# Performance work log

Hardware: AMD Instinct MI355X
Metric: run time of the kernel (lower is better)

## Reference

```python
import jax, jax.numpy as jnp
import numpy as np

B, S, H = 16, 4096, 512

def setup_inputs() -> dict:
    key = jax.random.key(0)
    k1, k2, k3, k4, k5 = jax.random.split(key, 5)
    hidden = jax.random.normal(k1, (B, H), dtype=jnp.float32)
    encoder_outputs = jax.random.normal(k2, (B, S, 2 * H), dtype=jnp.float32)
    # nn.Linear(3H, H): weight [H, 3H], bias [H]
    W_attn = jax.random.normal(k3, (H, 3 * H), dtype=jnp.float32) * (1.0 / np.sqrt(3 * H))
    b_attn = jax.random.normal(k4, (H,), dtype=jnp.float32) * 0.01
    v = jax.random.normal(k5, (H,), dtype=jnp.float32)
    return {"hidden": hidden, "encoder_outputs": encoder_outputs,
            "W_attn": W_attn, "b_attn": b_attn, "v": v}

def reference(hidden, encoder_outputs, W_attn, b_attn, v):
    src_len = encoder_outputs.shape[1]
    # [B, S, H] broadcast of decoder hidden, concat with encoder outputs -> [B, S, 3H]
    h_rep = jnp.broadcast_to(hidden[:, None, :], (hidden.shape[0], src_len, hidden.shape[1]))
    combined = jnp.concatenate([h_rep, encoder_outputs], axis=2)
    energy = jnp.tanh(jnp.einsum('bsf,hf->bsh', combined, W_attn) + b_attn)
    attention = jnp.einsum('bsh,h->bs', energy, v)  # bmm(v, energy.T) squeezed
    return jax.nn.softmax(attention, axis=1)
```

## Files before the change

### kernel.cpp

```cpp
#include <hip/hip_runtime.h>

typedef __attribute__((ext_vector_type(4))) float f32x4;
typedef __attribute__((ext_vector_type(8))) short bf16x8;
typedef __attribute__((ext_vector_type(4))) short bf16x4;

#define MEMBAR() asm volatile("" ::: "memory")

__device__ __forceinline__ unsigned short f2bf(float f) {
  unsigned int u = __builtin_bit_cast(unsigned int, f);
  u += 0x7FFFu + ((u >> 16) & 1u);
  return (unsigned short)(u >> 16);
}

__global__ __launch_bounds__(256) void k_prep(
    const float* __restrict__ W, const float* __restrict__ hidden,
    const float* __restrict__ bias, unsigned short* __restrict__ W2t,
    float* __restrict__ P) {
  __shared__ float hsh[512];
  const int bid = blockIdx.x;
  const int tid = threadIdx.x;
  if (bid < 256) {
    const int id = bid * 256 + tid;
    const int kk8 = (id & 3) * 8;
    const int h = (id >> 2) & 511;
    const int kb = id >> 11;
    const float* src = W + (long)h * 1536 + 512 + kb * 32 + kk8;
    float4 a = *reinterpret_cast<const float4*>(src);
    float4 c = *reinterpret_cast<const float4*>(src + 4);
    union { unsigned short u[8]; bf16x8 v; } o;
    o.u[0] = f2bf(a.x); o.u[1] = f2bf(a.y); o.u[2] = f2bf(a.z); o.u[3] = f2bf(a.w);
    o.u[4] = f2bf(c.x); o.u[5] = f2bf(c.y); o.u[6] = f2bf(c.z); o.u[7] = f2bf(c.w);
    *reinterpret_cast<bf16x8*>(W2t + (long)kb * 16384 + h * 32 + kk8) = o.v;
  } else {
    const int bid2 = bid - 256;
    const int b = bid2 >> 1;
    const int h = (bid2 & 1) * 256 + tid;
    for (int i = tid; i < 512; i += 256) hsh[i] = hidden[b * 512 + i];
    __syncthreads();
    const float* wr = W + (long)h * 1536;
    float s = 0.f;
#pragma unroll 4
    for (int f = 0; f < 512; f += 4) {
      float4 wv = *reinterpret_cast<const float4*>(wr + f);
      s += wv.x * hsh[f] + wv.y * hsh[f + 1] + wv.z * hsh[f + 2] + wv.w * hsh[f + 3];
    }
    P[b * 512 + h] = bias[h] + s;
  }
}

__global__ __launch_bounds__(512, 2) void k_main(
    const float* __restrict__ enc, const short* __restrict__ W2t,
    const float* __restrict__ P, const float* __restrict__ v,
    float* __restrict__ logits) {
  __shared__ short As[4][2048];
  __shared__ float attred[64][8];

  const int tid = threadIdx.x;
  const int lane = tid & 63;
  const int w = tid >> 6;
  const int hl = lane & 15, kg = lane >> 4;
  const long rowbase = (long)blockIdx.x * 64;
  const int b = (int)(rowbase >> 12);

  const int r = tid >> 3, c = tid & 7;
  const f32x4* gp = reinterpret_cast<const f32x4*>(enc + (rowbase + r) * 1024) + c;
  const int wr_off = r * 32 + ((((c >> 1) ^ ((r >> 1) & 3)) << 3)) + ((c & 1) << 2);
  const int base_f = hl * 32 + ((kg ^ ((hl >> 1) & 3)) << 3);
  const short* bp = W2t + (w * 64 + hl) * 32 + kg * 8;

  f32x4 acc[4][4];
#pragma unroll
  for (int mi = 0; mi < 4; ++mi)
#pragma unroll
    for (int ni = 0; ni < 4; ++ni) acc[mi][ni] = (f32x4){0.f, 0.f, 0.f, 0.f};

  bf16x8 Ba[4], Bb[4];
  f32x4 rawE, rawO;

#define CVT4W(BUF, RAW) {                                             \
    union { __bf16 h[4]; bf16x4 s; } _u;                              \
    _u.h[0] = (__bf16)(RAW)[0]; _u.h[1] = (__bf16)(RAW)[1];           \
    _u.h[2] = (__bf16)(RAW)[2]; _u.h[3] = (__bf16)(RAW)[3];           \
    *reinterpret_cast<bf16x4*>(&As[(BUF)][wr_off]) = _u.s;            \
  }
#define LOADB(DST, KB) {                                              \
    const short* _k = bp + (KB) * 16384;                              \
    DST[0] = *reinterpret_cast<const bf16x8*>(_k);                    \
    DST[1] = *reinterpret_cast<const bf16x8*>(_k + 512);              \
    DST[2] = *reinterpret_cast<const bf16x8*>(_k + 1024);             \
    DST[3] = *reinterpret_cast<const bf16x8*>(_k + 1536);             \
  }
#define K_ITER(J, RAWIN, RAWOUT, BIN, BOUT, DO_G, DO_B, DO_CVT) {     \
    MEMBAR();                                                         \
    __builtin_amdgcn_s_barrier();                                     \
    MEMBAR();                                                         \
    if (DO_G) RAWOUT = gp[((J) + 2) * 8];                             \
    if (DO_B) LOADB(BOUT, (J) + 1);                                   \
    MEMBAR();                                                         \
    const short* _ab = &As[(J) & 3][0];                               \
    bf16x8 _f0 = *reinterpret_cast<const bf16x8*>(_ab + base_f);      \
    bf16x8 _f1 = *reinterpret_cast<const bf16x8*>(_ab + base_f + 512);\
    bf16x8 _f2 = *reinterpret_cast<const bf16x8*>(_ab + base_f + 1024);\
    bf16x8 _f3 = *reinterpret_cast<const bf16x8*>(_ab + base_f + 1536);\
    acc[0][0] = __builtin_amdgcn_mfma_f32_16x16x32_bf16(_f0, BIN[0], acc[0][0], 0, 0, 0); \
    acc[0][1] = __builtin_amdgcn_mfma_f32_16x16x32_bf16(_f0, BIN[1], acc[0][1], 0, 0, 0); \
    acc[0][2] = __builtin_amdgcn_mfma_f32_16x16x32_bf16(_f0, BIN[2], acc[0][2], 0, 0, 0); \
    acc[0][3] = __builtin_amdgcn_mfma_f32_16x16x32_bf16(_f0, BIN[3], acc[0][3], 0, 0, 0); \
    acc[1][0] = __builtin_amdgcn_mfma_f32_16x16x32_bf16(_f1, BIN[0], acc[1][0], 0, 0, 0); \
    acc[1][1] = __builtin_amdgcn_mfma_f32_16x16x32_bf16(_f1, BIN[1], acc[1][1], 0, 0, 0); \
    acc[1][2] = __builtin_amdgcn_mfma_f32_16x16x32_bf16(_f1, BIN[2], acc[1][2], 0, 0, 0); \
    acc[1][3] = __builtin_amdgcn_mfma_f32_16x16x32_bf16(_f1, BIN[3], acc[1][3], 0, 0, 0); \
    acc[2][0] = __builtin_amdgcn_mfma_f32_16x16x32_bf16(_f2, BIN[0], acc[2][0], 0, 0, 0); \
    acc[2][1] = __builtin_amdgcn_mfma_f32_16x16x32_bf16(_f2, BIN[1], acc[2][1], 0, 0, 0); \
    acc[2][2] = __builtin_amdgcn_mfma_f32_16x16x32_bf16(_f2, BIN[2], acc[2][2], 0, 0, 0); \
    acc[2][3] = __builtin_amdgcn_mfma_f32_16x16x32_bf16(_f2, BIN[3], acc[2][3], 0, 0, 0); \
    acc[3][0] = __builtin_amdgcn_mfma_f32_16x16x32_bf16(_f3, BIN[0], acc[3][0], 0, 0, 0); \
    acc[3][1] = __builtin_amdgcn_mfma_f32_16x16x32_bf16(_f3, BIN[1], acc[3][1], 0, 0, 0); \
    acc[3][2] = __builtin_amdgcn_mfma_f32_16x16x32_bf16(_f3, BIN[2], acc[3][2], 0, 0, 0); \
    acc[3][3] = __builtin_amdgcn_mfma_f32_16x16x32_bf16(_f3, BIN[3], acc[3][3], 0, 0, 0); \
    if (DO_CVT) CVT4W(((J) + 1) & 3, RAWIN);                          \
    asm volatile("s_waitcnt lgkmcnt(0)" ::: "memory");                \
  }

  {
    f32x4 raw0 = gp[0];
    CVT4W(0, raw0);
  }
  rawO = gp[8];
  LOADB(Ba, 0);
  __syncthreads();

#pragma unroll 1
  for (int p = 0; p < 15; ++p) {
    const int j = p * 2;
    K_ITER(j,     rawO, rawE, Ba, Bb, 1, 1, 1);
    K_ITER(j + 1, rawE, rawO, Bb, Ba, 1, 1, 1);
  }
  K_ITER(30, rawO, rawE, Ba, Bb, 0, 1, 1);
  K_ITER(31, rawE, rawO, Bb, Ba, 0, 0, 0);

#undef K_ITER
#undef LOADB
#undef CVT4W

  float part[4][4];
#pragma unroll
  for (int mi = 0; mi < 4; ++mi)
#pragma unroll
    for (int rr = 0; rr < 4; ++rr) part[mi][rr] = 0.f;

#pragma unroll
  for (int ni = 0; ni < 4; ++ni) {
    const int h = w * 64 + ni * 16 + hl;
    const float ph = P[b * 512 + h];
    const float vh = v[h];
#pragma unroll
    for (int mi = 0; mi < 4; ++mi)
#pragma unroll
      for (int rr = 0; rr < 4; ++rr) {
        float x = acc[mi][ni][rr] + ph;
        float e = __expf(2.f * x);
        part[mi][rr] += vh * (1.f - 2.f * __frcp_rn(e + 1.f));
      }
  }
#pragma unroll
  for (int off = 1; off < 16; off <<= 1)
#pragma unroll
    for (int mi = 0; mi < 4; ++mi)
#pragma unroll
      for (int rr = 0; rr < 4; ++rr)
        part[mi][rr] += __shfl_xor(part[mi][rr], off, 16);

  if (hl == 0) {
#pragma unroll
    for (int mi = 0; mi < 4; ++mi)
#pragma unroll
      for (int rr = 0; rr < 4; ++rr)
        attred[mi * 16 + kg * 4 + rr][w] = part[mi][rr];
  }
  __syncthreads();
  if (tid < 64) {
    const float* a = attred[tid];
    logits[rowbase + tid] = ((a[0] + a[1]) + (a[2] + a[3])) +
                            ((a[4] + a[5]) + (a[6] + a[7]));
  }
}

__global__ __launch_bounds__(256) void k_softmax(
    const float* __restrict__ logits, float* __restrict__ out) {
  const int b = blockIdx.x;
  const int t = threadIdx.x;
  const int wid = t >> 6, lane = t & 63;
  const float* L = logits + b * 4096;
  __shared__ float rmax[4], rsum[4];
  float lv[16];
  float m = -1e30f;
#pragma unroll
  for (int i = 0; i < 16; ++i) {
    lv[i] = L[t + i * 256];
    m = fmaxf(m, lv[i]);
  }
#pragma unroll
  for (int off = 32; off >= 1; off >>= 1) m = fmaxf(m, __shfl_xor(m, off));
  if (lane == 0) rmax[wid] = m;
  __syncthreads();
  m = fmaxf(fmaxf(rmax[0], rmax[1]), fmaxf(rmax[2], rmax[3]));
  float s = 0.f;
#pragma unroll
  for (int i = 0; i < 16; ++i) {
    lv[i] = __expf(lv[i] - m);
    s += lv[i];
  }
#pragma unroll
  for (int off = 32; off >= 1; off >>= 1) s += __shfl_xor(s, off);
  if (lane == 0) rsum[wid] = s;
  __syncthreads();
  s = rsum[0] + rsum[1] + rsum[2] + rsum[3];
  float inv = 1.0f / s;
#pragma unroll
  for (int i = 0; i < 16; ++i) out[b * 4096 + t + i * 256] = lv[i] * inv;
}

extern "C" void kernel_launch(void* const* d_in, const int* in_sizes, int n_in,
                              void* d_out, int out_size, void* d_ws, size_t ws_size,
                              hipStream_t stream) {
  const float* hidden = (const float*)d_in[0];
  const float* enc    = (const float*)d_in[1];
  const float* W      = (const float*)d_in[2];
  const float* bias   = (const float*)d_in[3];
  const float* v      = (const float*)d_in[4];
  float* out = (float*)d_out;

  char* ws = (char*)d_ws;
  float* P = (float*)ws;
  unsigned short* W2t = (unsigned short*)(ws + 32768);
  float* logits = (float*)(ws + 32768 + 1048576);

  k_prep<<<288, 256, 0, stream>>>(W, hidden, bias, W2t, P);
  k_main<<<1024, 512, 0, stream>>>(enc, (const short*)W2t, P, v, logits);
  k_softmax<<<16, 256, 0, stream>>>(logits, out);
}
```

Measured before the change: 121.1 us.

## Load encoder A fragments directly from global memory into registers, bypassing LDS

```diff
diff --git a/kernel.cpp b/kernel.cpp
--- a/kernel.cpp
+++ b/kernel.cpp
@@ -2,7 +2,6 @@
 
 typedef __attribute__((ext_vector_type(4))) float f32x4;
 typedef __attribute__((ext_vector_type(8))) short bf16x8;
-typedef __attribute__((ext_vector_type(4))) short bf16x4;
 
 #define MEMBAR() asm volatile("" ::: "memory")
 
@@ -52,7 +51,6 @@
     const float* __restrict__ enc, const short* __restrict__ W2t,
     const float* __restrict__ P, const float* __restrict__ v,
     float* __restrict__ logits) {
-  __shared__ short As[4][2048];
   __shared__ float attred[64][8];
 
   const int tid = threadIdx.x;
@@ -62,10 +60,11 @@
   const long rowbase = (long)blockIdx.x * 64;
   const int b = (int)(rowbase >> 12);
 
-  const int r = tid >> 3, c = tid & 7;
-  const f32x4* gp = reinterpret_cast<const f32x4*>(enc + (rowbase + r) * 1024) + c;
-  const int wr_off = r * 32 + ((((c >> 1) ^ ((r >> 1) & 3)) << 3)) + ((c & 1) << 2);
-  const int base_f = hl * 32 + ((kg ^ ((hl >> 1) & 3)) << 3);
+  const f32x4* ap[4];
+#pragma unroll
+  for (int mi = 0; mi < 4; ++mi)
+    ap[mi] = reinterpret_cast<const f32x4*>(enc + (rowbase + mi * 16 + hl) * 1024 +
+                                            kg * 8);
   const short* bp = W2t + (w * 64 + hl) * 32 + kg * 8;
 
   f32x4 acc[4][4];
@@ -74,15 +73,10 @@
 #pragma unroll
     for (int ni = 0; ni < 4; ++ni) acc[mi][ni] = (f32x4){0.f, 0.f, 0.f, 0.f};
 
-  bf16x8 Ba[4], Bb[4];
-  f32x4 rawE, rawO;
-
-#define CVT4W(BUF, RAW) {                                             \
-    union { __bf16 h[4]; bf16x4 s; } _u;                              \
-    _u.h[0] = (__bf16)(RAW)[0]; _u.h[1] = (__bf16)(RAW)[1];           \
-    _u.h[2] = (__bf16)(RAW)[2]; _u.h[3] = (__bf16)(RAW)[3];           \
-    *reinterpret_cast<bf16x4*>(&As[(BUF)][wr_off]) = _u.s;            \
-  }
+  f32x4 s0[8], s1[8], s2[8];
+  bf16x8 af[4];
+  bf16x8 b0[4], b1[4];
+
 #define LOADB(DST, KB) {                                              \
     const short* _k = bp + (KB) * 16384;                              \
     DST[0] = *reinterpret_cast<const bf16x8*>(_k);                    \
@@ -90,58 +84,73 @@
     DST[2] = *reinterpret_cast<const bf16x8*>(_k + 1024);             \
     DST[3] = *reinterpret_cast<const bf16x8*>(_k + 1536);             \
   }
-#define K_ITER(J, RAWIN, RAWOUT, BIN, BOUT, DO_G, DO_B, DO_CVT) {     \
+#define LOADA(SET, T) {                                               \
+    _Pragma("unroll") for (int mi = 0; mi < 4; ++mi) {                \
+      SET[2 * mi]     = ap[mi][(T) * 8];                              \
+      SET[2 * mi + 1] = ap[mi][(T) * 8 + 1];                          \
+    }                                                                 \
+  }
+#define CVTA(SET) {                                                   \
+    _Pragma("unroll") for (int mi = 0; mi < 4; ++mi) {                \
+      f32x4 _lo = SET[2 * mi], _hi = SET[2 * mi + 1];                 \
+      union { __bf16 h[8]; bf16x8 s; } _u;                            \
+      _u.h[0] = (__bf16)_lo[0]; _u.h[1] = (__bf16)_lo[1];             \
+      _u.h[2] = (__bf16)_lo[2]; _u.h[3] = (__bf16)_lo[3];             \
+      _u.h[4] = (__bf16)_hi[0]; _u.h[5] = (__bf16)_hi[1];             \
+      _u.h[6] = (__bf16)_hi[2]; _u.h[7] = (__bf16)_hi[3];             \
+      af[mi] = _u.s;                                                  \
+    }                                                                 \
+  }
+#define MFMA16(BS) {                                                  \
+    _Pragma("unroll") for (int mi = 0; mi < 4; ++mi) {                \
+      acc[mi][0] = __builtin_amdgcn_mfma_f32_16x16x32_bf16(af[mi], BS[0], acc[mi][0], 0, 0, 0); \
+      acc[mi][1] = __builtin_amdgcn_mfma_f32_16x16x32_bf16(af[mi], BS[1], acc[mi][1], 0, 0, 0); \
+      acc[mi][2] = __builtin_amdgcn_mfma_f32_16x16x32_bf16(af[mi], BS[2], acc[mi][2], 0, 0, 0); \
+      acc[mi][3] = __builtin_amdgcn_mfma_f32_16x16x32_bf16(af[mi], BS[3], acc[mi][3], 0, 0, 0); \
+    }                                                                 \
+  }
+#define K_IT(J, SLD, SCVT, BUSE, BLD, DO_GA, DO_GB, DO_CVT) {         \
+    if (DO_GB) LOADB(BLD, (J) + 1);                                   \
+    if (DO_GA) LOADA(SLD, (J) + 3);                                   \
     MEMBAR();                                                         \
-    __builtin_amdgcn_s_barrier();                                     \
+    MFMA16(BUSE)                                                      \
     MEMBAR();                                                         \
-    if (DO_G) RAWOUT = gp[((J) + 2) * 8];                             \
-    if (DO_B) LOADB(BOUT, (J) + 1);                                   \
+    if (DO_CVT) CVTA(SCVT);                                           \
     MEMBAR();                                                         \
-    const short* _ab = &As[(J) & 3][0];                               \
-    bf16x8 _f0 = *reinterpret_cast<const bf16x8*>(_ab + base_f);      \
-    bf16x8 _f1 = *reinterpret_cast<const bf16x8*>(_ab + base_f + 512);\
-    bf16x8 _f2 = *reinterpret_cast<const bf16x8*>(_ab + base_f + 1024);\
-    bf16x8 _f3 = *reinterpret_cast<const bf16x8*>(_ab + base_f + 1536);\
-    acc[0][0] = __builtin_amdgcn_mfma_f32_16x16x32_bf16(_f0, BIN[0], acc[0][0], 0, 0, 0); \
-    acc[0][1] = __builtin_amdgcn_mfma_f32_16x16x32_bf16(_f0, BIN[1], acc[0][1], 0, 0, 0); \
-    acc[0][2] = __builtin_amdgcn_mfma_f32_16x16x32_bf16(_f0, BIN[2], acc[0][2], 0, 0, 0); \
-    acc[0][3] = __builtin_amdgcn_mfma_f32_16x16x32_bf16(_f0, BIN[3], acc[0][3], 0, 0, 0); \
-    acc[1][0] = __builtin_amdgcn_mfma_f32_16x16x32_bf16(_f1, BIN[0], acc[1][0], 0, 0, 0); \
-    acc[1][1] = __builtin_amdgcn_mfma_f32_16x16x32_bf16(_f1, BIN[1], acc[1][1], 0, 0, 0); \
-    acc[1][2] = __builtin_amdgcn_mfma_f32_16x16x32_bf16(_f1, BIN[2], acc[1][2], 0, 0, 0); \
-    acc[1][3] = __builtin_amdgcn_mfma_f32_16x16x32_bf16(_f1, BIN[3], acc[1][3], 0, 0, 0); \
-    acc[2][0] = __builtin_amdgcn_mfma_f32_16x16x32_bf16(_f2, BIN[0], acc[2][0], 0, 0, 0); \
-    acc[2][1] = __builtin_amdgcn_mfma_f32_16x16x32_bf16(_f2, BIN[1], acc[2][1], 0, 0, 0); \
-    acc[2][2] = __builtin_amdgcn_mfma_f32_16x16x32_bf16(_f2, BIN[2], acc[2][2], 0, 0, 0); \
-    acc[2][3] = __builtin_amdgcn_mfma_f32_16x16x32_bf16(_f2, BIN[3], acc[2][3], 0, 0, 0); \
-    acc[3][0] = __builtin_amdgcn_mfma_f32_16x16x32_bf16(_f3, BIN[0], acc[3][0], 0, 0, 0); \
-    acc[3][1] = __builtin_amdgcn_mfma_f32_16x16x32_bf16(_f3, BIN[1], acc[3][1], 0, 0, 0); \
-    acc[3][2] = __builtin_amdgcn_mfma_f32_16x16x32_bf16(_f3, BIN[2], acc[3][2], 0, 0, 0); \
-    acc[3][3] = __builtin_amdgcn_mfma_f32_16x16x32_bf16(_f3, BIN[3], acc[3][3], 0, 0, 0); \
-    if (DO_CVT) CVT4W(((J) + 1) & 3, RAWIN);                          \
-    asm volatile("s_waitcnt lgkmcnt(0)" ::: "memory");                \
-  }
-
-  {
-    f32x4 raw0 = gp[0];
-    CVT4W(0, raw0);
-  }
-  rawO = gp[8];
-  LOADB(Ba, 0);
-  __syncthreads();
+  }
+
+  LOADB(b0, 0);
+  LOADA(s0, 0);
+  LOADA(s1, 1);
+  LOADA(s2, 2);
+  MEMBAR();
+  CVTA(s0);
+  MEMBAR();
 
 #pragma unroll 1
-  for (int p = 0; p < 15; ++p) {
-    const int j = p * 2;
-    K_ITER(j,     rawO, rawE, Ba, Bb, 1, 1, 1);
-    K_ITER(j + 1, rawE, rawO, Bb, Ba, 1, 1, 1);
-  }
-  K_ITER(30, rawO, rawE, Ba, Bb, 0, 1, 1);
-  K_ITER(31, rawE, rawO, Bb, Ba, 0, 0, 0);
-
-#undef K_ITER
+  for (int p = 0; p < 4; ++p) {
+    const int j = p * 6;
+    K_IT(j + 0, s0, s1, b0, b1, 1, 1, 1)
+    K_IT(j + 1, s1, s2, b1, b0, 1, 1, 1)
+    K_IT(j + 2, s2, s0, b0, b1, 1, 1, 1)
+    K_IT(j + 3, s0, s1, b1, b0, 1, 1, 1)
+    K_IT(j + 4, s1, s2, b0, b1, 1, 1, 1)
+    K_IT(j + 5, s2, s0, b1, b0, 1, 1, 1)
+  }
+  K_IT(24, s0, s1, b0, b1, 1, 1, 1)
+  K_IT(25, s1, s2, b1, b0, 1, 1, 1)
+  K_IT(26, s2, s0, b0, b1, 1, 1, 1)
+  K_IT(27, s0, s1, b1, b0, 1, 1, 1)
+  K_IT(28, s1, s2, b0, b1, 1, 1, 1)
+  K_IT(29, s2, s0, b1, b0, 0, 1, 1)
+  K_IT(30, s0, s1, b0, b1, 0, 1, 1)
+  K_IT(31, s1, s2, b1, b0, 0, 0, 0)
+
+#undef K_IT
+#undef MFMA16
+#undef CVTA
+#undef LOADA
 #undef LOADB
-#undef CVT4W
 
   float part[4][4];
 #pragma unroll
```

New measurement: 347.5 us. 187% more time.
